# Kernel tuning notes

Measured on AMD Instinct MI355X. Metric: run time of the kernel, lower is better.

## Reference

```python
import jax, jax.numpy as jnp
import numpy as np

N, M = 1024, 64          # n nodes, window size m
B = 8                    # batch
FN = FE = 64             # input feature dims (nodes/edges)
AN = AE = 64             # aggregated feature dims
ON = OE = 64             # output dims (module bug: node path uses bias_edges/activation_edges, so ON must equal OE)


def _indices():
    w = np.minimum(np.arange(N), M)                      # window size per node i: min(i, m)
    node_start = np.concatenate([[0], np.cumsum(w)[:-1]]).astype(np.int64)  # first edge id of node i
    E = int(w.sum())                                     # total edges = 63456
    dst = np.repeat(np.arange(N), w)                     # edge k -> target node i
    pos = np.arange(E) - np.repeat(node_start, w)        # edge k -> position t within node i's window
    src = dst - w[dst] + pos                             # edge k -> source node j = j0 + t, j0 = i - min(i,m)
    return w, node_start, E, dst, pos, src


def setup_inputs() -> dict:
    key = jax.random.key(0)
    ks = jax.random.split(key, 13)
    _, _, E, _, _, _ = _indices()
    u = lambda k, shape: jax.random.uniform(k, shape, jnp.float32, -0.1, 0.1)
    return {
        "input_nodes": jax.random.normal(ks[0], (B, N, FN), jnp.float32),
        "input_edges": jax.random.normal(ks[1], (B, E, FE), jnp.float32),
        # node-aggregation MLP: cat(node_j, node_i, edge) -> 2*AN -> AN  (ReLU only after 2nd linear)
        "Wn1": u(ks[2], (2 * FN + FE, 2 * AN)), "bn1": u(ks[3], (2 * AN,)),
        "Wn2": u(ks[4], (2 * AN, AN)),          "bn2": u(ks[5], (AN,)),
        # edge-aggregation MLP: cat(node_j, edge) -> 2*AE -> AE
        "We1": u(ks[6], (FN + FE, 2 * AE)),     "be1": u(ks[7], (2 * AE,)),
        "We2": u(ks[8], (2 * AE, AE)),          "be2": u(ks[9], (AE,)),
        # output projections (exclude_last=False -> concat agg with last input)
        "W_nodes": u(ks[10], (AN + FN, ON)),
        "W_edges": u(ks[11], (AE + FE, OE)),
        "bias_edges": u(ks[12], (OE,)),          # used by BOTH node and edge outputs (source-code bug)
    }


def reference(input_nodes, input_edges, Wn1, bn1, Wn2, bn2, We1, be1, We2, be2,
              W_nodes, W_edges, bias_edges):
    w_np, node_start, E, dst, pos, src = _indices()
    relu = jax.nn.relu

    nodes_src = input_nodes[:, src]                      # [B,E,FN] node j of edge k
    nodes_dst = input_nodes[:, dst]                      # [B,E,FN] node i of edge k (the 'last' node)

    # Per-pair aggregation MLPs (NO activation between linears, matching source)
    pair_e = relu((jnp.concatenate([nodes_src, input_edges], -1) @ We1 + be1) @ We2 + be2)            # [B,E,AE]
    pair_n = relu((jnp.concatenate([nodes_src, nodes_dst, input_edges], -1) @ Wn1 + bn1) @ Wn2 + bn2)  # [B,E,AN]

    # ---- node aggregation: mean of pair_n over each node's full window (zeros if window empty) ----
    w = jnp.asarray(w_np)
    agg_n = jnp.zeros((B, N, AN), pair_n.dtype).at[:, dst].add(pair_n)
    agg_n = agg_n / jnp.maximum(w, 1)[None, :, None]     # w=0 -> sum is 0 -> zeros, matches torch

    # ---- edge aggregation: prefix mean within each node's window (pairs t < pos(k)) ----
    t = np.arange(M)
    k_pad = node_start[:, None] + t[None, :]             # [N,M] flat edge id of pair t of node i
    valid = t[None, :] < w_np[:, None]
    k_pad = np.where(valid, k_pad, 0)
    pair_pad = pair_e[:, k_pad.reshape(-1)].reshape(B, N, M, AE)
    pair_pad = pair_pad * jnp.asarray(valid, pair_e.dtype).reshape(1, N, M, 1)
    csum = jnp.cumsum(pair_pad, axis=2)                  # inclusive prefix sums over window positions
    prefix = jnp.concatenate([jnp.zeros_like(csum[:, :, :1]), csum[:, :, :-1]], axis=2)  # exclusive
    pos_j = jnp.asarray(pos)
    mean_e = prefix[:, dst, pos_j] / jnp.maximum(pos_j, 1)[None, :, None]  # [B,E,AE]; pos=0 -> zeros

    # ---- output projections (exclude_last=False). Node path uses bias_edges + edge activation (bug). ----
    out_edges = relu(jnp.concatenate([mean_e, input_edges], -1) @ W_edges + bias_edges)   # [B,E,OE]
    out_nodes = relu(jnp.concatenate([agg_n, input_nodes], -1) @ W_nodes + bias_edges)    # [B,N,ON]
    return out_nodes, out_edges
```

## Files before the change

kernel.cpp:

```cpp
#include <hip/hip_runtime.h>

#define NN 1024
#define MM 64
#define BB 8
#define EE 63456

#define WS_WN    0
#define WS_WE    12288
#define WS_BN    20480
#define WS_BE    20544
#define WS_B2H   20608
#define WS_B2L   28800
#define WS_B5H   36992
#define WS_B5L   41088
#define WS_TOTAL 45184

using short8 = __attribute__((ext_vector_type(8))) short;
using f32x16 = __attribute__((ext_vector_type(16))) float;

__device__ __forceinline__ unsigned bf16_rne(float x) {
    unsigned u = __float_as_uint(x);
    return (u + 0x7fffu + ((u >> 16) & 1u)) >> 16;
}

__global__ __launch_bounds__(64)
void collapse_kernel(
    const float* __restrict__ Wn1, const float* __restrict__ bn1,
    const float* __restrict__ Wn2, const float* __restrict__ bn2,
    const float* __restrict__ We1, const float* __restrict__ be1,
    const float* __restrict__ We2, const float* __restrict__ be2,
    float* __restrict__ ws)
{
    const int r = blockIdx.x;
    const int n = threadIdx.x;
    if (r < 192) {
        float acc = 0.f;
#pragma unroll 16
        for (int t = 0; t < 128; ++t) acc += Wn1[r * 128 + t] * Wn2[t * 64 + n];
        ws[WS_WN + r * 64 + n] = acc;
    } else if (r < 320) {
        const int rr = r - 192;
        float acc = 0.f;
#pragma unroll 16
        for (int t = 0; t < 128; ++t) acc += We1[rr * 128 + t] * We2[t * 64 + n];
        ws[WS_WE + rr * 64 + n] = acc;
    } else if (r == 320) {
        float acc = bn2[n];
#pragma unroll 16
        for (int t = 0; t < 128; ++t) acc += bn1[t] * Wn2[t * 64 + n];
        ws[WS_BN + n] = acc;
    } else {
        float acc = be2[n];
#pragma unroll 16
        for (int t = 0; t < 128; ++t) acc += be1[t] * We2[t * 64 + n];
        ws[WS_BE + n] = acc;
    }
}

__global__ void pack_kernel(const float* __restrict__ Wef, float* __restrict__ ws)
{
    int idx = blockIdx.x * 256 + threadIdx.x;
    if (idx >= 24576) return;
    float v; int pos, offh, offl;
    if (idx < 16384) {
        int e = idx & 7, l = (idx >> 3) & 63, ks = (idx >> 9) & 7, nt = idx >> 12;
        int k = ks * 16 + (l >> 5) * 8 + e;
        int n = nt * 32 + (l & 31);
        if (n < 64) {
            int r = (k < 64) ? k : (64 + k);
            v = ws[WS_WN + r * 64 + n];
        } else {
            v = ws[WS_WE + k * 64 + (n - 64)];
        }
        pos = idx; offh = WS_B2H; offl = WS_B2L;
    } else {
        int t2 = idx - 16384;
        int e = t2 & 7, l = (t2 >> 3) & 63, ks = (t2 >> 9) & 7, nt = t2 >> 12;
        int k = ks * 16 + (l >> 5) * 8 + e;
        int n = nt * 32 + (l & 31);
        v = Wef[k * 64 + n];
        pos = t2; offh = WS_B5H; offl = WS_B5L;
    }
    unsigned hh = bf16_rne(v);
    unsigned ll = bf16_rne(v - __uint_as_float(hh << 16));
    ((unsigned short*)(ws + offh))[pos] = (unsigned short)hh;
    ((unsigned short*)(ws + offl))[pos] = (unsigned short)ll;
}

__global__ __launch_bounds__(512, 4)
void main_kernel(const float* __restrict__ nodes,
                 const float* __restrict__ edges,
                 const float* __restrict__ ws,
                 const float* __restrict__ Wnf,
                 const float* __restrict__ bias,
                 float* __restrict__ out)
{
    __shared__ __align__(16) unsigned short s_A[64 * 128];
    __shared__ float s_red[3 * 64];
    __shared__ float s_dd[64];
    __shared__ float s_dst[64];
    __shared__ float s_gn[4 * 64];

    const int tid = threadIdx.x;
    const int bx  = blockIdx.x;
    const int b   = bx >> 10;
    const int i   = bx & 1023;
    const int w   = (i < MM) ? i : MM;
    const long ns_ = (i <= 64) ? ((long)i * (i - 1)) / 2 : 2016L + (long)(i - 64) * 64;

    const int wv = tid >> 6, l = tid & 63, lo5 = l & 31, hi = l >> 5;
    const int mt = wv & 1;

    short8 pbh[8], pbl[8];
    {
        const int slab = wv >> 1;
        const unsigned short* Bh = (const unsigned short*)(ws + WS_B2H);
        const unsigned short* Bl = (const unsigned short*)(ws + WS_B2L);
#pragma unroll
        for (int ks = 0; ks < 8; ++ks) {
            pbh[ks] = *(const short8*)&Bh[((slab * 8 + ks) * 64 + l) * 8];
            pbl[ks] = *(const short8*)&Bl[((slab * 8 + ks) * 64 + l) * 8];
        }
    }

    if (tid < 16)
        *(float4*)&s_dst[tid * 4] = ((const float4*)(nodes + ((size_t)b * NN + i) * 64))[tid];
    for (int idx = tid; idx < w * 16; idx += 512) {
        const int row = idx >> 4, q = idx & 15;
        const float* src = (q < 8)
            ? (nodes + ((size_t)b * NN + (i - w) + row) * 64 + q * 8)
            : (edges + ((size_t)b * EE + ns_ + row) * 64 + (q - 8) * 8);
        float4 x0 = *(const float4*)src;
        float4 x1 = *(const float4*)(src + 4);
        unsigned h0 = bf16_rne(x0.x), h1 = bf16_rne(x0.y), h2 = bf16_rne(x0.z), h3 = bf16_rne(x0.w);
        unsigned h4 = bf16_rne(x1.x), h5 = bf16_rne(x1.y), h6 = bf16_rne(x1.z), h7 = bf16_rne(x1.w);
        uint4 H;
        H.x = h0 | (h1 << 16); H.y = h2 | (h3 << 16);
        H.z = h4 | (h5 << 16); H.w = h6 | (h7 << 16);
        *(uint4*)&s_A[row * 128 + (q ^ (row & 15)) * 8] = H;
    }
    __syncthreads();

    if (wv == 0) {
        float acc = ws[WS_BN + l];
#pragma unroll 8
        for (int c = 0; c < 64; ++c) acc += s_dst[c] * ws[WS_WN + (64 + c) * 64 + l];
        s_dd[l] = acc;
    }

    f32x16 acc = {};
    {
        const int r = mt * 32 + lo5;
#pragma unroll
        for (int ks = 0; ks < 8; ++ks) {
            const int u = ks * 2 + hi;
            short8 a = *(const short8*)&s_A[r * 128 + (u ^ (r & 15)) * 8];
            acc = __builtin_amdgcn_mfma_f32_32x32x16_bf16(a, pbh[ks], acc, 0, 0, 0);
            acc = __builtin_amdgcn_mfma_f32_32x32x16_bf16(a, pbl[ks], acc, 0, 0, 0);
        }
    }

    short8 qbh[4], qbl[4];
    const int ntc = (wv >> 1) & 1;
    const int dup = wv >> 2;
    {
        const unsigned short* Bh = (const unsigned short*)(ws + WS_B5H);
        const unsigned short* Bl = (const unsigned short*)(ws + WS_B5L);
        const int k0 = dup ? 4 : 0;
#pragma unroll
        for (int kk = 0; kk < 4; ++kk) {
            const int ks = k0 + kk;
            qbh[kk] = *(const short8*)&Bh[((ntc * 8 + ks) * 64 + l) * 8];
            qbl[kk] = *(const short8*)&Bl[((ntc * 8 + ks) * 64 + l) * 8];
        }
    }
    __syncthreads();

    if (wv < 4) {
        const int f = (wv >> 1) * 32 + lo5;
        const float dd = s_dd[f];
        float sum = 0.f;
#pragma unroll
        for (int reg = 0; reg < 16; ++reg) {
            const int r = mt * 32 + (reg & 3) + 8 * (reg >> 2) + 4 * hi;
            if (r < w) sum += fmaxf(acc[reg] + dd, 0.f);
        }
        sum += __shfl_xor(sum, 32);
        if (hi == 0) s_red[mt * 64 + f] = sum;
    } else {
        const int fp = ((wv >> 1) - 2) * 32 + lo5;
        const float be = ws[WS_BE + fp];
        const int uoff = fp >> 3, foff = fp & 7;
#pragma unroll
        for (int reg = 0; reg < 16; ++reg) {
            const int j = mt * 32 + (reg & 3) + 8 * (reg >> 2) + 4 * hi;
            float p = (j < w) ? fmaxf(acc[reg] + be, 0.f) : 0.f;
            s_A[j * 128 + (uoff ^ (j & 15)) * 8 + foff] = (unsigned short)bf16_rne(p);
        }
    }
    __syncthreads();

    float* s_ze = (float*)s_A;
    const int rbase = mt * 32;
    f32x16 z = {};
    {
        const int r = rbase + lo5;
        const int k0 = dup ? 4 : 0;
#pragma unroll
        for (int kk = 0; kk < 4; ++kk) {
            const int u = (k0 + kk) * 2 + hi;
            short8 a = *(const short8*)&s_A[r * 128 + (u ^ (r & 15)) * 8];
            z = __builtin_amdgcn_mfma_f32_32x32x16_bf16(a, qbh[kk], z, 0, 0, 0);
            z = __builtin_amdgcn_mfma_f32_32x32x16_bf16(a, qbl[kk], z, 0, 0, 0);
        }
    }

    float pz[16], base[4], cbase = 0.f;
    if (!dup) {
        float G[4];
#pragma unroll
        for (int g = 0; g < 4; ++g) {
            float a0 = z[g * 4 + 0], a1 = z[g * 4 + 1], a2 = z[g * 4 + 2], a3 = z[g * 4 + 3];
            pz[g * 4 + 0] = 0.f;
            pz[g * 4 + 1] = a0;
            pz[g * 4 + 2] = a0 + a1;
            pz[g * 4 + 3] = a0 + a1 + a2;
            G[g] = a0 + a1 + a2 + a3;
        }
        float Gp[4];
#pragma unroll
        for (int g = 0; g < 4; ++g) Gp[g] = __shfl_xor(G[g], 32);
        float run = 0.f;
#pragma unroll
        for (int g = 0; g < 4; ++g) {
            const float g0 = hi ? Gp[g] : G[g];
            base[g] = run + (hi ? g0 : 0.f);
            run += G[g] + Gp[g];
        }
        if (mt == 0 && hi == 0) s_red[128 + ntc * 32 + lo5] = run;
    } else {
        const int q = tid - 256, f = q & 63, p = q >> 6;
        const float invw = 1.0f / (float)((w > 0) ? w : 1);
        float s = 0.f;
#pragma unroll 4
        for (int c = p * 16; c < p * 16 + 16; ++c) {
            const float aggc = (s_red[c] + s_red[64 + c]) * invw;
            s += aggc * Wnf[c * 64 + f] + s_dst[c] * Wnf[(64 + c) * 64 + f];
        }
        s_gn[p * 64 + f] = s;
    }
    __syncthreads();

    if (dup) {
#pragma unroll
        for (int reg = 0; reg < 16; ++reg) {
            const int j = rbase + (reg & 3) + 8 * (reg >> 2) + 4 * hi;
            s_ze[j * 64 + ntc * 32 + lo5] = z[reg];
        }
    }
    __syncthreads();

    if (!dup) {
        if (mt == 1) cbase = s_red[128 + ntc * 32 + lo5];
        const int f = ntc * 32 + lo5;
        const float bv = bias[f];
        float* oute = out + (size_t)BB * NN * 64;
#pragma unroll
        for (int reg = 0; reg < 16; ++reg) {
            const int j = rbase + (reg & 3) + 8 * (reg >> 2) + 4 * hi;
            if (j < w) {
                const float invj = (j > 0) ? (1.0f / (float)j) : 1.0f;
                const float zev = s_ze[j * 64 + f];
                oute[((size_t)b * EE + ns_ + j) * 64 + f] =
                    fmaxf((cbase + base[reg >> 2] + pz[reg]) * invj + zev + bv, 0.f);
            }
        }
    } else if (wv == 4 && l < 64) {
        const float a2 = bias[l] + s_gn[l] + s_gn[64 + l] + s_gn[128 + l] + s_gn[192 + l];
        out[((size_t)b * NN + i) * 64 + l] = fmaxf(a2, 0.f);
    }
}

extern "C" void kernel_launch(void* const* d_in, const int* in_sizes, int n_in,
                              void* d_out, int out_size, void* d_ws, size_t ws_size,
                              hipStream_t stream) {
    const float* nodes = (const float*)d_in[0];
    const float* edges = (const float*)d_in[1];
    const float* Wn1  = (const float*)d_in[2];
    const float* bn1  = (const float*)d_in[3];
    const float* Wn2  = (const float*)d_in[4];
    const float* bn2  = (const float*)d_in[5];
    const float* We1  = (const float*)d_in[6];
    const float* be1  = (const float*)d_in[7];
    const float* We2  = (const float*)d_in[8];
    const float* be2  = (const float*)d_in[9];
    const float* Wnod = (const float*)d_in[10];
    const float* Wedg = (const float*)d_in[11];
    const float* bias = (const float*)d_in[12];
    float* ws = (float*)d_ws;
    float* out = (float*)d_out;

    hipLaunchKernelGGL(collapse_kernel, dim3(322), dim3(64), 0, stream,
                       Wn1, bn1, Wn2, bn2, We1, be1, We2, be2, ws);
    hipLaunchKernelGGL(pack_kernel, dim3(96), dim3(256), 0, stream, Wedg, ws);
    hipLaunchKernelGGL(main_kernel, dim3(BB * NN), dim3(512), 0, stream,
                       nodes, edges, ws, Wnod, bias, out);
}
```

Baseline: 367.9 us.

## Halve block to 256 threads with each wave computing both row tiles

The main kernel block drops from 512 to 256 threads. Each wave now handles both 32-row M tiles, so each B fragment loaded into registers serves two MFMA chains instead of being duplicated across waves. The pair activations move to a separate LDS buffer, so the second GEMM can overlap with the edge-side partial product over s_A. The node output reduction is restructured to use shuffles, which removes one barrier and the s_gn and s_red scratch. This raises per-thread register pressure (two accumulators per GEMM) in exchange for fewer threads, less duplicated weight loading, and more blocks per CU.

```diff
diff --git a/kernel.cpp b/kernel.cpp
--- a/kernel.cpp
+++ b/kernel.cpp
@@ -87,7 +87,7 @@
     ((unsigned short*)(ws + offl))[pos] = (unsigned short)ll;
 }
 
-__global__ __launch_bounds__(512, 4)
+__global__ __launch_bounds__(256, 6)
 void main_kernel(const float* __restrict__ nodes,
                  const float* __restrict__ edges,
                  const float* __restrict__ ws,
@@ -96,10 +96,10 @@
                  float* __restrict__ out)
 {
     __shared__ __align__(16) unsigned short s_A[64 * 128];
-    __shared__ float s_red[3 * 64];
-    __shared__ float s_dd[64];
+    __shared__ __align__(16) unsigned short s_pair[64 * 64];
+    __shared__ float s_dd[4 * 64];
+    __shared__ float s_agg[64];
     __shared__ float s_dst[64];
-    __shared__ float s_gn[4 * 64];
 
     const int tid = threadIdx.x;
     const int bx  = blockIdx.x;
@@ -109,23 +109,36 @@
     const long ns_ = (i <= 64) ? ((long)i * (i - 1)) / 2 : 2016L + (long)(i - 64) * 64;
 
     const int wv = tid >> 6, l = tid & 63, lo5 = l & 31, hi = l >> 5;
-    const int mt = wv & 1;
+    const bool nw = wv < 2;
+    const int ntc = nw ? wv : (wv - 2);
 
     short8 pbh[8], pbl[8];
     {
-        const int slab = wv >> 1;
         const unsigned short* Bh = (const unsigned short*)(ws + WS_B2H);
         const unsigned short* Bl = (const unsigned short*)(ws + WS_B2L);
 #pragma unroll
         for (int ks = 0; ks < 8; ++ks) {
-            pbh[ks] = *(const short8*)&Bh[((slab * 8 + ks) * 64 + l) * 8];
-            pbl[ks] = *(const short8*)&Bl[((slab * 8 + ks) * 64 + l) * 8];
-        }
-    }
+            pbh[ks] = *(const short8*)&Bh[((wv * 8 + ks) * 64 + l) * 8];
+            pbl[ks] = *(const short8*)&Bl[((wv * 8 + ks) * 64 + l) * 8];
+        }
+    }
+    short8 qbh[4], qbl[4];
+    {
+        const unsigned short* Bh = (const unsigned short*)(ws + WS_B5H);
+        const unsigned short* Bl = (const unsigned short*)(ws + WS_B5L);
+        const int k0 = nw ? 0 : 4;
+#pragma unroll
+        for (int kk = 0; kk < 4; ++kk) {
+            qbh[kk] = *(const short8*)&Bh[((ntc * 8 + k0 + kk) * 64 + l) * 8];
+            qbl[kk] = *(const short8*)&Bl[((ntc * 8 + k0 + kk) * 64 + l) * 8];
+        }
+    }
+    const float bnv = nw ? ws[WS_BN + wv * 32 + lo5] : ws[WS_BE + ntc * 32 + lo5];
+    const float bsv = bias[ntc * 32 + lo5];
 
     if (tid < 16)
         *(float4*)&s_dst[tid * 4] = ((const float4*)(nodes + ((size_t)b * NN + i) * 64))[tid];
-    for (int idx = tid; idx < w * 16; idx += 512) {
+    for (int idx = tid; idx < w * 16; idx += 256) {
         const int row = idx >> 4, q = idx & 15;
         const float* src = (q < 8)
             ? (nodes + ((size_t)b * NN + (i - w) + row) * 64 + q * 8)
@@ -141,143 +154,162 @@
     }
     __syncthreads();
 
-    if (wv == 0) {
-        float acc = ws[WS_BN + l];
-#pragma unroll 8
-        for (int c = 0; c < 64; ++c) acc += s_dst[c] * ws[WS_WN + (64 + c) * 64 + l];
-        s_dd[l] = acc;
-    }
-
-    f32x16 acc = {};
     {
-        const int r = mt * 32 + lo5;
+        float a = 0.f;
+        const float* wd = ws + WS_WN + 64 * 64;
+#pragma unroll
+        for (int cc = 0; cc < 16; ++cc) {
+            const int c = wv * 16 + cc;
+            a += s_dst[c] * wd[c * 64 + l];
+        }
+        s_dd[wv * 64 + l] = a;
+    }
+
+    f32x16 acc0 = {}, acc1 = {};
+    const int r0 = lo5, r1 = 32 + lo5;
+    {
 #pragma unroll
         for (int ks = 0; ks < 8; ++ks) {
             const int u = ks * 2 + hi;
-            short8 a = *(const short8*)&s_A[r * 128 + (u ^ (r & 15)) * 8];
-            acc = __builtin_amdgcn_mfma_f32_32x32x16_bf16(a, pbh[ks], acc, 0, 0, 0);
-            acc = __builtin_amdgcn_mfma_f32_32x32x16_bf16(a, pbl[ks], acc, 0, 0, 0);
-        }
-    }
-
-    short8 qbh[4], qbl[4];
-    const int ntc = (wv >> 1) & 1;
-    const int dup = wv >> 2;
-    {
-        const unsigned short* Bh = (const unsigned short*)(ws + WS_B5H);
-        const unsigned short* Bl = (const unsigned short*)(ws + WS_B5L);
-        const int k0 = dup ? 4 : 0;
+            short8 a0 = *(const short8*)&s_A[r0 * 128 + (u ^ (r0 & 15)) * 8];
+            short8 a1 = *(const short8*)&s_A[r1 * 128 + (u ^ (r1 & 15)) * 8];
+            acc0 = __builtin_amdgcn_mfma_f32_32x32x16_bf16(a0, pbh[ks], acc0, 0, 0, 0);
+            acc0 = __builtin_amdgcn_mfma_f32_32x32x16_bf16(a0, pbl[ks], acc0, 0, 0, 0);
+            acc1 = __builtin_amdgcn_mfma_f32_32x32x16_bf16(a1, pbh[ks], acc1, 0, 0, 0);
+            acc1 = __builtin_amdgcn_mfma_f32_32x32x16_bf16(a1, pbl[ks], acc1, 0, 0, 0);
+        }
+    }
+
+    if (!nw) {
+        const int fp = ntc * 32 + lo5, ufp = fp >> 3, fo = fp & 7;
+#pragma unroll
+        for (int reg = 0; reg < 16; ++reg) {
+            const int rr = (reg & 3) + 8 * (reg >> 2) + 4 * hi;
+            {
+                float p = (rr < w) ? fmaxf(acc0[reg] + bnv, 0.f) : 0.f;
+                s_pair[rr * 64 + ((ufp ^ (rr & 7)) << 3) + fo] = (unsigned short)bf16_rne(p);
+            }
+            {
+                const int j2 = 32 + rr;
+                float p = (j2 < w) ? fmaxf(acc1[reg] + bnv, 0.f) : 0.f;
+                s_pair[j2 * 64 + ((ufp ^ (j2 & 7)) << 3) + fo] = (unsigned short)bf16_rne(p);
+            }
+        }
+    }
+    __syncthreads();
+
+    if (nw) {
+        const int f = wv * 32 + lo5;
+        const float dd = bnv + s_dd[f] + s_dd[64 + f] + s_dd[128 + f] + s_dd[192 + f];
+        float sum = 0.f;
+#pragma unroll
+        for (int reg = 0; reg < 16; ++reg) {
+            const int rr = (reg & 3) + 8 * (reg >> 2) + 4 * hi;
+            if (rr < w)      sum += fmaxf(acc0[reg] + dd, 0.f);
+            if (32 + rr < w) sum += fmaxf(acc1[reg] + dd, 0.f);
+        }
+        sum += __shfl_xor(sum, 32);
+        if (hi == 0) s_agg[f] = sum;
+    }
+
+    f32x16 z0 = {}, z1 = {};
+    if (nw) {
 #pragma unroll
         for (int kk = 0; kk < 4; ++kk) {
-            const int ks = k0 + kk;
-            qbh[kk] = *(const short8*)&Bh[((ntc * 8 + ks) * 64 + l) * 8];
-            qbl[kk] = *(const short8*)&Bl[((ntc * 8 + ks) * 64 + l) * 8];
+            const int ku = kk * 2 + hi;
+            short8 a0 = *(const short8*)&s_pair[r0 * 64 + ((ku ^ (r0 & 7)) << 3)];
+            short8 a1 = *(const short8*)&s_pair[r1 * 64 + ((ku ^ (r1 & 7)) << 3)];
+            z0 = __builtin_amdgcn_mfma_f32_32x32x16_bf16(a0, qbh[kk], z0, 0, 0, 0);
+            z0 = __builtin_amdgcn_mfma_f32_32x32x16_bf16(a0, qbl[kk], z0, 0, 0, 0);
+            z1 = __builtin_amdgcn_mfma_f32_32x32x16_bf16(a1, qbh[kk], z1, 0, 0, 0);
+            z1 = __builtin_amdgcn_mfma_f32_32x32x16_bf16(a1, qbl[kk], z1, 0, 0, 0);
+        }
+    } else {
+#pragma unroll
+        for (int kk = 0; kk < 4; ++kk) {
+            const int u = (4 + kk) * 2 + hi;
+            short8 a0 = *(const short8*)&s_A[r0 * 128 + (u ^ (r0 & 15)) * 8];
+            short8 a1 = *(const short8*)&s_A[r1 * 128 + (u ^ (r1 & 15)) * 8];
+            z0 = __builtin_amdgcn_mfma_f32_32x32x16_bf16(a0, qbh[kk], z0, 0, 0, 0);
+            z0 = __builtin_amdgcn_mfma_f32_32x32x16_bf16(a0, qbl[kk], z0, 0, 0, 0);
+            z1 = __builtin_amdgcn_mfma_f32_32x32x16_bf16(a1, qbh[kk], z1, 0, 0, 0);
+            z1 = __builtin_amdgcn_mfma_f32_32x32x16_bf16(a1, qbl[kk], z1, 0, 0, 0);
         }
     }
     __syncthreads();
 
-    if (wv < 4) {
-        const int f = (wv >> 1) * 32 + lo5;
-        const float dd = s_dd[f];
-        float sum = 0.f;
+    float* s_ze = (float*)s_A;
+    float pz0[16], pz1[16], base0[4], base1[4], tot0 = 0.f;
+    if (nw) {
+        float G[4];
+#pragma unroll
+        for (int g = 0; g < 4; ++g) {
+            float a0 = z0[g * 4], a1 = z0[g * 4 + 1], a2 = z0[g * 4 + 2], a3 = z0[g * 4 + 3];
+            pz0[g * 4] = 0.f; pz0[g * 4 + 1] = a0; pz0[g * 4 + 2] = a0 + a1; pz0[g * 4 + 3] = a0 + a1 + a2;
+            G[g] = a0 + a1 + a2 + a3;
+        }
+        float run = 0.f;
+#pragma unroll
+        for (int g = 0; g < 4; ++g) {
+            float Gp = __shfl_xor(G[g], 32);
+            base0[g] = run + (hi ? Gp : 0.f);
+            run += G[g] + Gp;
+        }
+        tot0 = run;
+#pragma unroll
+        for (int g = 0; g < 4; ++g) {
+            float a0 = z1[g * 4], a1 = z1[g * 4 + 1], a2 = z1[g * 4 + 2], a3 = z1[g * 4 + 3];
+            pz1[g * 4] = 0.f; pz1[g * 4 + 1] = a0; pz1[g * 4 + 2] = a0 + a1; pz1[g * 4 + 3] = a0 + a1 + a2;
+            G[g] = a0 + a1 + a2 + a3;
+        }
+        run = 0.f;
+#pragma unroll
+        for (int g = 0; g < 4; ++g) {
+            float Gp = __shfl_xor(G[g], 32);
+            base1[g] = run + (hi ? Gp : 0.f);
+            run += G[g] + Gp;
+        }
+    } else {
+        const int fz = ntc * 32 + lo5;
 #pragma unroll
         for (int reg = 0; reg < 16; ++reg) {
-            const int r = mt * 32 + (reg & 3) + 8 * (reg >> 2) + 4 * hi;
-            if (r < w) sum += fmaxf(acc[reg] + dd, 0.f);
-        }
-        sum += __shfl_xor(sum, 32);
-        if (hi == 0) s_red[mt * 64 + f] = sum;
-    } else {
-        const int fp = ((wv >> 1) - 2) * 32 + lo5;
-        const float be = ws[WS_BE + fp];
-        const int uoff = fp >> 3, foff = fp & 7;
+            const int rr = (reg & 3) + 8 * (reg >> 2) + 4 * hi;
+            s_ze[rr * 64 + fz]        = z0[reg];
+            s_ze[(32 + rr) * 64 + fz] = z1[reg];
+        }
+    }
+    __syncthreads();
+
+    if (nw) {
+        const int f = ntc * 32 + lo5;
+        float* oute = out + (size_t)BB * NN * 64;
 #pragma unroll
         for (int reg = 0; reg < 16; ++reg) {
-            const int j = mt * 32 + (reg & 3) + 8 * (reg >> 2) + 4 * hi;
-            float p = (j < w) ? fmaxf(acc[reg] + be, 0.f) : 0.f;
-            s_A[j * 128 + (uoff ^ (j & 15)) * 8 + foff] = (unsigned short)bf16_rne(p);
-        }
-    }
-    __syncthreads();
-
-    float* s_ze = (float*)s_A;
-    const int rbase = mt * 32;
-    f32x16 z = {};
-    {
-        const int r = rbase + lo5;
-        const int k0 = dup ? 4 : 0;
-#pragma unroll
-        for (int kk = 0; kk < 4; ++kk) {
-            const int u = (k0 + kk) * 2 + hi;
-            short8 a = *(const short8*)&s_A[r * 128 + (u ^ (r & 15)) * 8];
-            z = __builtin_amdgcn_mfma_f32_32x32x16_bf16(a, qbh[kk], z, 0, 0, 0);
-            z = __builtin_amdgcn_mfma_f32_32x32x16_bf16(a, qbl[kk], z, 0, 0, 0);
-        }
-    }
-
-    float pz[16], base[4], cbase = 0.f;
-    if (!dup) {
-        float G[4];
-#pragma unroll
-        for (int g = 0; g < 4; ++g) {
-            float a0 = z[g * 4 + 0], a1 = z[g * 4 + 1], a2 = z[g * 4 + 2], a3 = z[g * 4 + 3];
-            pz[g * 4 + 0] = 0.f;
-            pz[g * 4 + 1] = a0;
-            pz[g * 4 + 2] = a0 + a1;
-            pz[g * 4 + 3] = a0 + a1 + a2;
-            G[g] = a0 + a1 + a2 + a3;
-        }
-        float Gp[4];
-#pragma unroll
-        for (int g = 0; g < 4; ++g) Gp[g] = __shfl_xor(G[g], 32);
-        float run = 0.f;
-#pragma unroll
-        for (int g = 0; g < 4; ++g) {
-            const float g0 = hi ? Gp[g] : G[g];
-            base[g] = run + (hi ? g0 : 0.f);
-            run += G[g] + Gp[g];
-        }
-        if (mt == 0 && hi == 0) s_red[128 + ntc * 32 + lo5] = run;
-    } else {
-        const int q = tid - 256, f = q & 63, p = q >> 6;
+            const int rr = (reg & 3) + 8 * (reg >> 2) + 4 * hi;
+            if (rr < w) {
+                const float invj = (rr > 0) ? (1.0f / (float)rr) : 1.0f;
+                oute[((size_t)b * EE + ns_ + rr) * 64 + f] =
+                    fmaxf((base0[reg >> 2] + pz0[reg]) * invj + s_ze[rr * 64 + f] + bsv, 0.f);
+            }
+            const int j2 = 32 + rr;
+            if (j2 < w) {
+                const float invj = 1.0f / (float)j2;
+                oute[((size_t)b * EE + ns_ + j2) * 64 + f] =
+                    fmaxf((tot0 + base1[reg >> 2] + pz1[reg]) * invj + s_ze[j2 * 64 + f] + bsv, 0.f);
+            }
+        }
+    } else {
+        const int f = ntc * 32 + lo5;
         const float invw = 1.0f / (float)((w > 0) ? w : 1);
         float s = 0.f;
-#pragma unroll 4
-        for (int c = p * 16; c < p * 16 + 16; ++c) {
-            const float aggc = (s_red[c] + s_red[64 + c]) * invw;
-            s += aggc * Wnf[c * 64 + f] + s_dst[c] * Wnf[(64 + c) * 64 + f];
-        }
-        s_gn[p * 64 + f] = s;
-    }
-    __syncthreads();
-
-    if (dup) {
-#pragma unroll
-        for (int reg = 0; reg < 16; ++reg) {
-            const int j = rbase + (reg & 3) + 8 * (reg >> 2) + 4 * hi;
-            s_ze[j * 64 + ntc * 32 + lo5] = z[reg];
-        }
-    }
-    __syncthreads();
-
-    if (!dup) {
-        if (mt == 1) cbase = s_red[128 + ntc * 32 + lo5];
-        const int f = ntc * 32 + lo5;
-        const float bv = bias[f];
-        float* oute = out + (size_t)BB * NN * 64;
-#pragma unroll
-        for (int reg = 0; reg < 16; ++reg) {
-            const int j = rbase + (reg & 3) + 8 * (reg >> 2) + 4 * hi;
-            if (j < w) {
-                const float invj = (j > 0) ? (1.0f / (float)j) : 1.0f;
-                const float zev = s_ze[j * 64 + f];
-                oute[((size_t)b * EE + ns_ + j) * 64 + f] =
-                    fmaxf((cbase + base[reg >> 2] + pz[reg]) * invj + zev + bv, 0.f);
-            }
-        }
-    } else if (wv == 4 && l < 64) {
-        const float a2 = bias[l] + s_gn[l] + s_gn[64 + l] + s_gn[128 + l] + s_gn[192 + l];
-        out[((size_t)b * NN + i) * 64 + l] = fmaxf(a2, 0.f);
+#pragma unroll 8
+        for (int cc = 0; cc < 32; ++cc) {
+            const int c = hi * 32 + cc;
+            s += (s_agg[c] * invw) * Wnf[c * 64 + f] + s_dst[c] * Wnf[(64 + c) * 64 + f];
+        }
+        s += __shfl_xor(s, 32);
+        if (hi == 0)
+            out[((size_t)b * NN + i) * 64 + f] = fmaxf(s + bsv, 0.f);
     }
 }
 
@@ -303,6 +335,6 @@
     hipLaunchKernelGGL(collapse_kernel, dim3(322), dim3(64), 0, stream,
                        Wn1, bn1, Wn2, bn2, We1, be1, We2, be2, ws);
     hipLaunchKernelGGL(pack_kernel, dim3(96), dim3(256), 0, stream, Wedg, ws);
-    hipLaunchKernelGGL(main_kernel, dim3(BB * NN), dim3(512), 0, stream,
+    hipLaunchKernelGGL(main_kernel, dim3(BB * NN), dim3(256), 0, stream,
                        nodes, edges, ws, Wnod, bias, out);
 }
```

New measurement: 509.7 us. 1.39x slower.
